# Kernel optimization log

Measured on AMD Instinct MI355X. Metric: run time of the kernel, lower is better.

Reference implementation:

```python
import jax, jax.numpy as jnp
import numpy as np

B, T, N = 1024, 128, 5
HIDDEN = 160
FML = HIDDEN // N            # 32, per-node state width
FC = (256, 256, 512)
IN_F = (FML + 1) * N         # 165: full graph -> every node sees all 5 nodes
N_CLASSES = 7
BN_EPS = 1e-5


def setup_inputs() -> dict:
    key = jax.random.key(0)
    ks = jax.random.split(key, 12)
    init = lambda k, sh: (jax.random.normal(k, sh, jnp.float32) * 0.02)
    return {
        "x": jax.random.normal(ks[0], (B, N, T), jnp.float32),
        # per-node 3-layer MLP f_i, stacked over nodes
        "Wf1": init(ks[1], (N, IN_F, FC[0])), "bf1": jnp.zeros((N, FC[0]), jnp.float32),
        "Wf2": init(ks[2], (N, FC[0], FC[1])), "bf2": jnp.zeros((N, FC[1]), jnp.float32),
        "Wf3": init(ks[3], (N, FC[1], FML)), "bf3": jnp.zeros((N, FML), jnp.float32),
        # output head: Linear -> ReLU -> BatchNorm1d -> Linear -> Softmax
        "Wo1": init(ks[4], (IN_F, FC[2])), "bo1": jnp.zeros((FC[2],), jnp.float32),
        "gamma": jnp.ones((FC[2],), jnp.float32), "beta": jnp.zeros((FC[2],), jnp.float32),
        "Wo2": init(ks[5], (FC[2], N_CLASSES)), "bo2": jnp.zeros((N_CLASSES,), jnp.float32),
    }


def reference(x, Wf1, bf1, Wf2, bf2, Wf3, bf3, Wo1, bo1, gamma, beta, Wo2, bo2):
    batch = x.shape[0]
    xt = jnp.transpose(x, (2, 0, 1))                  # [T, B, N]
    state0 = jnp.zeros((batch, N, FML), x.dtype)      # [B, N, FML]

    def step(state, x_t):
        # Gauss-Seidel update: node i sees states already updated this step
        for i in range(N):
            inp = jnp.concatenate([x_t, state.reshape(batch, -1)], axis=1)  # [B, 165]
            h = jax.nn.relu(inp @ Wf1[i] + bf1[i])
            h = jax.nn.relu(h @ Wf2[i] + bf2[i])
            s_i = jax.nn.relu(h @ Wf3[i] + bf3[i])    # [B, FML]
            state = state.at[:, i, :].set(s_i)
        return state, None

    state, _ = jax.lax.scan(step, state0, xt)
    feat = jnp.concatenate([xt[-1], state.reshape(batch, -1)], axis=1)       # [B, 165]
    h = jax.nn.relu(feat @ Wo1 + bo1)
    # BatchNorm1d in training mode: batch mean, biased batch variance
    mu = jnp.mean(h, axis=0)
    var = jnp.mean((h - mu) ** 2, axis=0)
    h = (h - mu) / jnp.sqrt(var + BN_EPS) * gamma + beta
    logits = h @ Wo2 + bo2
    return jax.nn.softmax(logits, axis=1)             # [B, 7]
```

## Files before the change

kernel.cpp:

```cpp
#include <hip/hip_runtime.h>
#include <hip/hip_bf16.h>

#define B_TOT 1024
#define T_STEPS 128
#define N_NODES 5
#define FML 32
#define IN_F 165
#define F1 256
#define F2 256
#define F3 512
#define NCLS 7
#define BM 16
#define BMH 8

typedef __attribute__((ext_vector_type(8))) short bfrag;
typedef __attribute__((ext_vector_type(4))) float f32x4;

#define MFMA16 __builtin_amdgcn_mfma_f32_16x16x32_bf16

#define P1_NODE 43008
#define P1_XOFF 40960
#define L2_FRAGS 128
#define P2_NODE (L2_FRAGS * 64 * 8)
#define L3_FRAGS 16
#define P3_NODE (L3_FRAGS * 64 * 8)

#define INP_STRIDE 200
#define H_STRIDE 264

__device__ __forceinline__ __hip_bfloat16 tobf(float v) { return __float2bfloat16(v); }

__device__ __forceinline__ void phase_barrier() {
  asm volatile("s_waitcnt lgkmcnt(0)" ::: "memory");
  __builtin_amdgcn_s_barrier();
  __builtin_amdgcn_sched_barrier(0);
}

__global__ __launch_bounds__(256) void pack_weights(
    const float* __restrict__ Wf1, const float* __restrict__ Wf2, const float* __restrict__ Wf3,
    __hip_bfloat16* __restrict__ p1, __hip_bfloat16* __restrict__ p2, __hip_bfloat16* __restrict__ p3) {
  const int stride = gridDim.x * 256;
  for (int it = blockIdx.x * 256 + threadIdx.x; it < N_NODES * 14592; it += stride) {
    int node = it / 14592, u = it % 14592;
    if (u < 5120) {
      int lane = u & 63, frag = u >> 6;
      int kt = frag >> 4, ct = frag & 15;
      int g = lane >> 4, c16 = lane & 15;
      __hip_bfloat16* dst = p1 + (size_t)node * P1_NODE + (size_t)u * 8;
      const float* W = Wf1 + (size_t)node * IN_F * F1;
#pragma unroll
      for (int e = 0; e < 8; ++e) {
        int k = kt * 32 + g * 8 + e;
        dst[e] = tobf(W[(size_t)(5 + k) * F1 + ct * 16 + c16]);
      }
    } else if (u < 5376) {
      int v = u - 5120;
      int ct = v >> 4, c16 = v & 15;
      __hip_bfloat16* dst = p1 + (size_t)node * P1_NODE + P1_XOFF + (size_t)v * 8;
      const float* W = Wf1 + (size_t)node * IN_F * F1;
#pragma unroll
      for (int e = 0; e < 8; ++e)
        dst[e] = (e < 5) ? tobf(W[(size_t)e * F1 + ct * 16 + c16]) : tobf(0.f);
    } else if (u < 5376 + 8192) {
      int v = u - 5376;
      int lane = v & 63, frag = v >> 6;
      int kt = frag >> 4, ct = frag & 15;
      int g = lane >> 4, c16 = lane & 15;
      __hip_bfloat16* dst = p2 + (size_t)node * P2_NODE + (size_t)v * 8;
      const float* W = Wf2 + (size_t)node * F1 * F2;
#pragma unroll
      for (int e = 0; e < 8; ++e) {
        int k = kt * 32 + g * 8 + e;
        dst[e] = tobf(W[(size_t)k * F2 + ct * 16 + c16]);
      }
    } else {
      int v = u - 13568;
      int lane = v & 63, frag = v >> 6;
      int kt = frag >> 1, ct = frag & 1;
      int g = lane >> 4, c16 = lane & 15;
      __hip_bfloat16* dst = p3 + (size_t)node * P3_NODE + (size_t)v * 8;
      const float* W = Wf3 + (size_t)node * F2 * FML;
#pragma unroll
      for (int e = 0; e < 8; ++e) {
        int k = kt * 32 + g * 8 + e;
        dst[e] = tobf(W[(size_t)k * FML + ct * 16 + c16]);
      }
    }
  }
}

__device__ __forceinline__ void relu_pack_store(__hip_bfloat16* p, f32x4 acc, float4 b) {
  union { ushort4 v; __hip_bfloat16 h[4]; } u;
  u.h[0] = tobf(fmaxf(acc[0] + b.x, 0.f));
  u.h[1] = tobf(fmaxf(acc[1] + b.y, 0.f));
  u.h[2] = tobf(fmaxf(acc[2] + b.z, 0.f));
  u.h[3] = tobf(fmaxf(acc[3] + b.w, 0.f));
  *reinterpret_cast<ushort4*>(p) = u.v;
}

__global__ __launch_bounds__(1024, 4) void recur_kernel(
    const float* __restrict__ x,
    const __hip_bfloat16* __restrict__ p1, const float* __restrict__ bf1,
    const __hip_bfloat16* __restrict__ p2, const float* __restrict__ bf2,
    const __hip_bfloat16* __restrict__ p3, const float* __restrict__ bf3,
    float* __restrict__ feat_out) {
  __shared__ __align__(16) __hip_bfloat16 inp_s[BM][INP_STRIDE];
  __shared__ __align__(16) __hip_bfloat16 h1_s[BM][H_STRIDE];
  __shared__ __align__(16) __hip_bfloat16 h2_s[BM][H_STRIDE];
  __shared__ __align__(16) bfrag wf3_s[N_NODES * L3_FRAGS * 64];

  const int tid = threadIdx.x;
  const int lane = tid & 63;
  const int w = tid >> 6;
  const int g = lane >> 4;
  const int c16 = lane & 15;
  const int ct = w;
  const int r0 = blockIdx.x * BM;

  const bfrag* Pf1 = (const bfrag*)p1;
  const bfrag* Pf2 = (const bfrag*)p2;

  {
    const uint4* src = (const uint4*)p3;
    uint4* dst = (uint4*)wf3_s;
    for (int i2 = tid; i2 < N_NODES * L3_FRAGS * 64; i2 += 1024) dst[i2] = src[i2];
  }
  for (int idx = tid; idx < BM * INP_STRIDE; idx += 1024)
    ((__hip_bfloat16*)inp_s)[idx] = tobf(0.f);
  __syncthreads();
  if (tid < BM * N_NODES) {
    int r = tid / N_NODES, n = tid % N_NODES;
    inp_s[r][160 + n] = tobf(x[(size_t)(r0 + r) * (N_NODES * T_STEPS) + n * T_STEPS]);
  }
  __syncthreads();

  bfrag wL1[5], wL1x;
#pragma unroll
  for (int kt = 0; kt < 5; ++kt)
    wL1[kt] = Pf1[(size_t)0 * (P1_NODE / 8) + (kt * 16 + ct) * 64 + lane];
  {
    bfrag z = {0,0,0,0,0,0,0,0};
    wL1x = (g == 0) ? Pf1[(size_t)0 * (P1_NODE / 8) + P1_XOFF / 8 + ct * 16 + c16] : z;
  }

#pragma unroll 1
  for (int t = 0; t < T_STEPS; ++t) {
#pragma unroll 1
    for (int i = 0; i < N_NODES; ++i) {
      const int inext = (i + 1 == N_NODES) ? 0 : i + 1;

      bfrag w2[8];
      {
        const bfrag* P = Pf2 + (size_t)i * L2_FRAGS * 64;
#pragma unroll
        for (int kt = 0; kt < 8; ++kt)
          w2[kt] = P[(kt * 16 + ct) * 64 + lane];
      }
      {
        float4 bia = *(const float4*)&bf1[i * F1 + ct * 16 + 4 * g];
        bfrag a[5], a5;
#pragma unroll
        for (int kt = 0; kt < 5; ++kt)
          a[kt] = *(const bfrag*)&inp_s[c16][kt * 32 + g * 8];
        a5 = *(const bfrag*)&inp_s[c16][160 + g * 8];
        f32x4 acc = {0.f,0.f,0.f,0.f}, accb = {0.f,0.f,0.f,0.f};
        acc  = MFMA16(wL1[0], a[0], acc,  0, 0, 0);
        accb = MFMA16(wL1[3], a[3], accb, 0, 0, 0);
        acc  = MFMA16(wL1[1], a[1], acc,  0, 0, 0);
        accb = MFMA16(wL1[4], a[4], accb, 0, 0, 0);
        acc  = MFMA16(wL1[2], a[2], acc,  0, 0, 0);
        accb = MFMA16(wL1x,   a5,   accb, 0, 0, 0);
        acc += accb;
        relu_pack_store(&h1_s[c16][ct * 16 + 4 * g], acc, bia);
      }
      phase_barrier();

      bfrag w1n[5], w1nx;
      {
        const bfrag* P = Pf1 + (size_t)inext * (P1_NODE / 8);
#pragma unroll
        for (int kt = 0; kt < 5; ++kt)
          w1n[kt] = P[(kt * 16 + ct) * 64 + lane];
        bfrag z = {0,0,0,0,0,0,0,0};
        w1nx = (g == 0) ? P[P1_XOFF / 8 + ct * 16 + c16] : z;
      }
      {
        float4 bib = *(const float4*)&bf2[i * F2 + ct * 16 + 4 * g];
        bfrag ab[8];
#pragma unroll
        for (int kt = 0; kt < 8; ++kt)
          ab[kt] = *(const bfrag*)&h1_s[c16][kt * 32 + g * 8];
        f32x4 acc = {0.f,0.f,0.f,0.f}, accb = {0.f,0.f,0.f,0.f};
#pragma unroll
        for (int kt = 0; kt < 4; ++kt) {
          acc  = MFMA16(w2[kt],     ab[kt],     acc,  0, 0, 0);
          accb = MFMA16(w2[kt + 4], ab[kt + 4], accb, 0, 0, 0);
        }
        acc += accb;
        relu_pack_store(&h2_s[c16][ct * 16 + 4 * g], acc, bib);
      }
      phase_barrier();

      if (w < 2) {
        bfrag ac[8], wc[8];
#pragma unroll
        for (int kt = 0; kt < 8; ++kt) {
          wc[kt] = wf3_s[((size_t)i * L3_FRAGS + kt * 2 + w) * 64 + lane];
          ac[kt] = *(const bfrag*)&h2_s[c16][kt * 32 + g * 8];
        }
        f32x4 acc = {0.f,0.f,0.f,0.f}, accb = {0.f,0.f,0.f,0.f};
#pragma unroll
        for (int kt = 0; kt < 4; ++kt) {
          acc  = MFMA16(wc[kt],     ac[kt],     acc,  0, 0, 0);
          accb = MFMA16(wc[kt + 4], ac[kt + 4], accb, 0, 0, 0);
        }
        acc += accb;
        const int sc = i * FML + w * 16 + 4 * g;
        float4 bic = *(const float4*)&bf3[sc];
        union { ushort4 v; __hip_bfloat16 h[4]; } u;
        float vs[4];
#pragma unroll
        for (int e = 0; e < 4; ++e) {
          vs[e] = fmaxf(acc[e] + ((const float*)&bic)[e], 0.f);
          u.h[e] = tobf(vs[e]);
        }
        *reinterpret_cast<ushort4*>(&inp_s[c16][sc]) = u.v;
        if (t == T_STEPS - 1) {
#pragma unroll
          for (int e = 0; e < 4; ++e)
            feat_out[(size_t)(r0 + c16) * IN_F + 5 + sc + e] = vs[e];
        }
      } else if (i == N_NODES - 1 && t + 1 < T_STEPS && tid >= 512 && tid < 512 + BM * N_NODES) {
        int xr = (tid - 512) / N_NODES, xn = (tid - 512) % N_NODES;
        float xv = x[(size_t)(r0 + xr) * (N_NODES * T_STEPS) + xn * T_STEPS + (t + 1)];
        inp_s[xr][160 + xn] = tobf(xv);
      }
      phase_barrier();

#pragma unroll
      for (int kt = 0; kt < 5; ++kt) wL1[kt] = w1n[kt];
      wL1x = w1nx;
    }
  }

  if (tid < BM * N_NODES) {
    int r = tid / N_NODES, n = tid % N_NODES;
    feat_out[(size_t)(r0 + r) * IN_F + n] =
        x[(size_t)(r0 + r) * (N_NODES * T_STEPS) + n * T_STEPS + (T_STEPS - 1)];
  }
}

__global__ __launch_bounds__(256) void head1_kernel(
    const float* __restrict__ feat, const float* __restrict__ Wo1,
    const float* __restrict__ bo1, float* __restrict__ H) {
  __shared__ __align__(16) float f[BMH][168];
  const int tid = threadIdx.x;
  const int r0 = blockIdx.x * BMH;
  for (int idx = tid; idx < BMH * 168; idx += 256) {
    int r = idx / 168, c = idx % 168;
    f[r][c] = (c < IN_F) ? feat[(size_t)(r0 + r) * IN_F + c] : 0.f;
  }
  __syncthreads();
  const int c0 = tid, c1 = tid + 256;
  float acc0[BMH], acc1[BMH];
#pragma unroll
  for (int r = 0; r < BMH; ++r) { acc0[r] = 0.f; acc1[r] = 0.f; }
  int k = 0;
  for (; k + 3 < IN_F; k += 4) {
    float w00 = Wo1[(k + 0) * F3 + c0], w01 = Wo1[(k + 0) * F3 + c1];
    float w10 = Wo1[(k + 1) * F3 + c0], w11 = Wo1[(k + 1) * F3 + c1];
    float w20 = Wo1[(k + 2) * F3 + c0], w21 = Wo1[(k + 2) * F3 + c1];
    float w30 = Wo1[(k + 3) * F3 + c0], w31 = Wo1[(k + 3) * F3 + c1];
#pragma unroll
    for (int r = 0; r < BMH; ++r) {
      float4 v = *reinterpret_cast<const float4*>(&f[r][k]);
      acc0[r] = fmaf(v.x, w00, acc0[r]); acc1[r] = fmaf(v.x, w01, acc1[r]);
      acc0[r] = fmaf(v.y, w10, acc0[r]); acc1[r] = fmaf(v.y, w11, acc1[r]);
      acc0[r] = fmaf(v.z, w20, acc0[r]); acc1[r] = fmaf(v.z, w21, acc1[r]);
      acc0[r] = fmaf(v.w, w30, acc0[r]); acc1[r] = fmaf(v.w, w31, acc1[r]);
    }
  }
  {
    float w0 = Wo1[164 * F3 + c0], w1 = Wo1[164 * F3 + c1];
#pragma unroll
    for (int r = 0; r < BMH; ++r) {
      acc0[r] = fmaf(f[r][164], w0, acc0[r]);
      acc1[r] = fmaf(f[r][164], w1, acc1[r]);
    }
  }
  float b0 = bo1[c0], b1 = bo1[c1];
#pragma unroll
  for (int r = 0; r < BMH; ++r) {
    H[(size_t)(r0 + r) * F3 + c0] = fmaxf(acc0[r] + b0, 0.f);
    H[(size_t)(r0 + r) * F3 + c1] = fmaxf(acc1[r] + b1, 0.f);
  }
}

__global__ __launch_bounds__(256) void bn_stats_kernel(
    const float* __restrict__ H, const float* __restrict__ gamma,
    const float* __restrict__ beta, float* __restrict__ ab) {
  const int c = blockIdx.x;
  const int tid = threadIdx.x;
  float sm = 0.f, q = 0.f;
  for (int r = tid; r < B_TOT; r += 256) {
    float v = H[(size_t)r * F3 + c];
    sm += v; q += v * v;
  }
  __shared__ float ls[256], lq[256];
  ls[tid] = sm; lq[tid] = q;
  __syncthreads();
  for (int off = 128; off; off >>= 1) {
    if (tid < off) { ls[tid] += ls[tid + off]; lq[tid] += lq[tid + off]; }
    __syncthreads();
  }
  if (tid == 0) {
    float mu = ls[0] * (1.f / B_TOT);
    float var = lq[0] * (1.f / B_TOT) - mu * mu;
    float inv = rsqrtf(var + 1e-5f);
    float a = gamma[c] * inv;
    ab[c] = a;
    ab[F3 + c] = beta[c] - mu * a;
  }
}

__global__ __launch_bounds__(256) void out_kernel(
    const float* __restrict__ H, const float* __restrict__ ab,
    const float* __restrict__ Wo2, const float* __restrict__ bo2,
    float* __restrict__ out) {
  const int wid = threadIdx.x >> 6, lane = threadIdx.x & 63;
  const int r = blockIdx.x * 4 + wid;
  float acc[NCLS];
#pragma unroll
  for (int j = 0; j < NCLS; ++j) acc[j] = 0.f;
  for (int k = lane; k < F3; k += 64) {
    float hv = H[(size_t)r * F3 + k] * ab[k] + ab[F3 + k];
#pragma unroll
    for (int j = 0; j < NCLS; ++j) acc[j] = fmaf(hv, Wo2[k * NCLS + j], acc[j]);
  }
#pragma unroll
  for (int j = 0; j < NCLS; ++j)
    for (int off = 32; off; off >>= 1) acc[j] += __shfl_xor(acc[j], off);
  if (lane == 0) {
    float lg[NCLS], mx = -1e30f;
#pragma unroll
    for (int j = 0; j < NCLS; ++j) { lg[j] = acc[j] + bo2[j]; mx = fmaxf(mx, lg[j]); }
    float sum = 0.f;
#pragma unroll
    for (int j = 0; j < NCLS; ++j) { lg[j] = __expf(lg[j] - mx); sum += lg[j]; }
    float inv = 1.f / sum;
#pragma unroll
    for (int j = 0; j < NCLS; ++j) out[(size_t)r * NCLS + j] = lg[j] * inv;
  }
}

extern "C" void kernel_launch(void* const* d_in, const int* in_sizes, int n_in,
                              void* d_out, int out_size, void* d_ws, size_t ws_size,
                              hipStream_t stream) {
  const float* x   = (const float*)d_in[0];
  const float* Wf1 = (const float*)d_in[1];
  const float* bf1 = (const float*)d_in[2];
  const float* Wf2 = (const float*)d_in[3];
  const float* bf2 = (const float*)d_in[4];
  const float* Wf3 = (const float*)d_in[5];
  const float* bf3 = (const float*)d_in[6];
  const float* Wo1 = (const float*)d_in[7];
  const float* bo1 = (const float*)d_in[8];
  const float* gamma = (const float*)d_in[9];
  const float* beta  = (const float*)d_in[10];
  const float* Wo2 = (const float*)d_in[11];
  const float* bo2 = (const float*)d_in[12];
  float* out = (float*)d_out;

  char* ws = (char*)d_ws;
  size_t off = 0;
  __hip_bfloat16* p1 = (__hip_bfloat16*)(ws + off); off += (size_t)N_NODES * P1_NODE * 2;
  __hip_bfloat16* p2 = (__hip_bfloat16*)(ws + off); off += (size_t)N_NODES * P2_NODE * 2;
  __hip_bfloat16* p3 = (__hip_bfloat16*)(ws + off); off += (size_t)N_NODES * P3_NODE * 2;
  float* feat = (float*)(ws + off); off += (size_t)B_TOT * IN_F * 4;
  float* H    = (float*)(ws + off); off += (size_t)B_TOT * F3 * 4;
  float* ab   = (float*)(ws + off); off += 2 * F3 * 4;

  pack_weights<<<285, 256, 0, stream>>>(Wf1, Wf2, Wf3, p1, p2, p3);
  recur_kernel<<<B_TOT / BM, 1024, 0, stream>>>(x, p1, bf1, p2, bf2, p3, bf3, feat);
  head1_kernel<<<B_TOT / BMH, 256, 0, stream>>>(feat, Wo1, bo1, H);
  bn_stats_kernel<<<F3, 256, 0, stream>>>(H, gamma, beta, ab);
  out_kernel<<<B_TOT / 4, 256, 0, stream>>>(H, ab, Wo2, bo2, out);
}
```

Measured before the change: 1.569 ms.

## Enlarge batch tile to 64 rows with 8 waves each computing two column tiles

The recurrent kernel now processes 64 batch rows per block with 512 threads, where each wave holds weight fragments for two output column tiles and reuses them across four 16-row tiles. This amortizes per-step global weight-fragment loads over four times as many rows, but cuts the grid from 64 to 16 blocks, leaving most CUs idle on a 256-CU GPU. Layer-3 weights are now read from global memory instead of staged in shared memory, and the custom phase barrier is replaced by __syncthreads.

Result: slower. 2.546 ms (+62.3%).

```diff
diff --git a/kernel.cpp b/kernel.cpp
--- a/kernel.cpp
+++ b/kernel.cpp
@@ -10,7 +10,8 @@
 #define F2 256
 #define F3 512
 #define NCLS 7
-#define BM 16
+#define BM 64
+#define NRT 4
 #define BMH 8
 
 typedef __attribute__((ext_vector_type(8))) short bfrag;
@@ -29,12 +30,6 @@
 #define H_STRIDE 264
 
 __device__ __forceinline__ __hip_bfloat16 tobf(float v) { return __float2bfloat16(v); }
-
-__device__ __forceinline__ void phase_barrier() {
-  asm volatile("s_waitcnt lgkmcnt(0)" ::: "memory");
-  __builtin_amdgcn_s_barrier();
-  __builtin_amdgcn_sched_barrier(0);
-}
 
 __global__ __launch_bounds__(256) void pack_weights(
     const float* __restrict__ Wf1, const float* __restrict__ Wf2, const float* __restrict__ Wf3,
@@ -98,7 +93,7 @@
   *reinterpret_cast<ushort4*>(p) = u.v;
 }
 
-__global__ __launch_bounds__(1024, 4) void recur_kernel(
+__global__ __launch_bounds__(512, 2) void recur_kernel(
     const float* __restrict__ x,
     const __hip_bfloat16* __restrict__ p1, const float* __restrict__ bf1,
     const __hip_bfloat16* __restrict__ p2, const float* __restrict__ bf2,
@@ -107,25 +102,20 @@
   __shared__ __align__(16) __hip_bfloat16 inp_s[BM][INP_STRIDE];
   __shared__ __align__(16) __hip_bfloat16 h1_s[BM][H_STRIDE];
   __shared__ __align__(16) __hip_bfloat16 h2_s[BM][H_STRIDE];
-  __shared__ __align__(16) bfrag wf3_s[N_NODES * L3_FRAGS * 64];
 
   const int tid = threadIdx.x;
   const int lane = tid & 63;
   const int w = tid >> 6;
   const int g = lane >> 4;
   const int c16 = lane & 15;
-  const int ct = w;
+  const int ct0 = 2 * w, ct1 = 2 * w + 1;
   const int r0 = blockIdx.x * BM;
 
   const bfrag* Pf1 = (const bfrag*)p1;
   const bfrag* Pf2 = (const bfrag*)p2;
-
-  {
-    const uint4* src = (const uint4*)p3;
-    uint4* dst = (uint4*)wf3_s;
-    for (int i2 = tid; i2 < N_NODES * L3_FRAGS * 64; i2 += 1024) dst[i2] = src[i2];
-  }
-  for (int idx = tid; idx < BM * INP_STRIDE; idx += 1024)
+  const bfrag* Pf3 = (const bfrag*)p3;
+
+  for (int idx = tid; idx < BM * INP_STRIDE; idx += 512)
     ((__hip_bfloat16*)inp_s)[idx] = tobf(0.f);
   __syncthreads();
   if (tid < BM * N_NODES) {
@@ -134,13 +124,16 @@
   }
   __syncthreads();
 
-  bfrag wL1[5], wL1x;
-#pragma unroll
-  for (int kt = 0; kt < 5; ++kt)
-    wL1[kt] = Pf1[(size_t)0 * (P1_NODE / 8) + (kt * 16 + ct) * 64 + lane];
+  bfrag wL1[2][5], wL1x[2];
+#pragma unroll
+  for (int kt = 0; kt < 5; ++kt) {
+    wL1[0][kt] = Pf1[(kt * 16 + ct0) * 64 + lane];
+    wL1[1][kt] = Pf1[(kt * 16 + ct1) * 64 + lane];
+  }
   {
     bfrag z = {0,0,0,0,0,0,0,0};
-    wL1x = (g == 0) ? Pf1[(size_t)0 * (P1_NODE / 8) + P1_XOFF / 8 + ct * 16 + c16] : z;
+    wL1x[0] = (g == 0) ? Pf1[P1_XOFF / 8 + ct0 * 16 + c16] : z;
+    wL1x[1] = (g == 0) ? Pf1[P1_XOFF / 8 + ct1 * 16 + c16] : z;
   }
 
 #pragma unroll 1
@@ -149,73 +142,110 @@
     for (int i = 0; i < N_NODES; ++i) {
       const int inext = (i + 1 == N_NODES) ? 0 : i + 1;
 
-      bfrag w2[8];
+      bfrag w2[2][8];
       {
         const bfrag* P = Pf2 + (size_t)i * L2_FRAGS * 64;
 #pragma unroll
-        for (int kt = 0; kt < 8; ++kt)
-          w2[kt] = P[(kt * 16 + ct) * 64 + lane];
+        for (int kt = 0; kt < 8; ++kt) {
+          w2[0][kt] = P[(kt * 16 + ct0) * 64 + lane];
+          w2[1][kt] = P[(kt * 16 + ct1) * 64 + lane];
+        }
       }
       {
-        float4 bia = *(const float4*)&bf1[i * F1 + ct * 16 + 4 * g];
-        bfrag a[5], a5;
-#pragma unroll
-        for (int kt = 0; kt < 5; ++kt)
-          a[kt] = *(const bfrag*)&inp_s[c16][kt * 32 + g * 8];
-        a5 = *(const bfrag*)&inp_s[c16][160 + g * 8];
-        f32x4 acc = {0.f,0.f,0.f,0.f}, accb = {0.f,0.f,0.f,0.f};
-        acc  = MFMA16(wL1[0], a[0], acc,  0, 0, 0);
-        accb = MFMA16(wL1[3], a[3], accb, 0, 0, 0);
-        acc  = MFMA16(wL1[1], a[1], acc,  0, 0, 0);
-        accb = MFMA16(wL1[4], a[4], accb, 0, 0, 0);
-        acc  = MFMA16(wL1[2], a[2], acc,  0, 0, 0);
-        accb = MFMA16(wL1x,   a5,   accb, 0, 0, 0);
-        acc += accb;
-        relu_pack_store(&h1_s[c16][ct * 16 + 4 * g], acc, bia);
-      }
-      phase_barrier();
-
-      bfrag w1n[5], w1nx;
+        float4 biA0 = *(const float4*)&bf1[i * F1 + ct0 * 16 + 4 * g];
+        float4 biA1 = *(const float4*)&bf1[i * F1 + ct1 * 16 + 4 * g];
+#pragma unroll
+        for (int rt = 0; rt < NRT; ++rt) {
+          const int row = rt * 16 + c16;
+          bfrag a[5], a5;
+#pragma unroll
+          for (int kt = 0; kt < 5; ++kt)
+            a[kt] = *(const bfrag*)&inp_s[row][kt * 32 + g * 8];
+          a5 = *(const bfrag*)&inp_s[row][160 + g * 8];
+          f32x4 acc0 = {0.f,0.f,0.f,0.f}, acc1 = {0.f,0.f,0.f,0.f};
+          f32x4 acc0b = {0.f,0.f,0.f,0.f}, acc1b = {0.f,0.f,0.f,0.f};
+#pragma unroll
+          for (int kt = 0; kt < 2; ++kt) {
+            acc0  = MFMA16(wL1[0][kt],     a[kt],     acc0,  0, 0, 0);
+            acc1  = MFMA16(wL1[1][kt],     a[kt],     acc1,  0, 0, 0);
+            acc0b = MFMA16(wL1[0][kt + 2], a[kt + 2], acc0b, 0, 0, 0);
+            acc1b = MFMA16(wL1[1][kt + 2], a[kt + 2], acc1b, 0, 0, 0);
+          }
+          acc0  = MFMA16(wL1[0][4], a[4], acc0,  0, 0, 0);
+          acc1  = MFMA16(wL1[1][4], a[4], acc1,  0, 0, 0);
+          acc0b = MFMA16(wL1x[0],   a5,   acc0b, 0, 0, 0);
+          acc1b = MFMA16(wL1x[1],   a5,   acc1b, 0, 0, 0);
+          acc0 += acc0b; acc1 += acc1b;
+          relu_pack_store(&h1_s[row][ct0 * 16 + 4 * g], acc0, biA0);
+          relu_pack_store(&h1_s[row][ct1 * 16 + 4 * g], acc1, biA1);
+        }
+      }
+      __syncthreads();
+
+      bfrag w1n[2][5], w1nx[2];
       {
         const bfrag* P = Pf1 + (size_t)inext * (P1_NODE / 8);
 #pragma unroll
-        for (int kt = 0; kt < 5; ++kt)
-          w1n[kt] = P[(kt * 16 + ct) * 64 + lane];
+        for (int kt = 0; kt < 5; ++kt) {
+          w1n[0][kt] = P[(kt * 16 + ct0) * 64 + lane];
+          w1n[1][kt] = P[(kt * 16 + ct1) * 64 + lane];
+        }
         bfrag z = {0,0,0,0,0,0,0,0};
-        w1nx = (g == 0) ? P[P1_XOFF / 8 + ct * 16 + c16] : z;
-      }
+        w1nx[0] = (g == 0) ? P[P1_XOFF / 8 + ct0 * 16 + c16] : z;
+        w1nx[1] = (g == 0) ? P[P1_XOFF / 8 + ct1 * 16 + c16] : z;
+      }
+      float xv = 0.f;
+      if (i == 4 && tid < BM * N_NODES && t + 1 < T_STEPS)
+        xv = x[(size_t)(r0 + tid / N_NODES) * (N_NODES * T_STEPS) +
+               (tid % N_NODES) * T_STEPS + (t + 1)];
       {
-        float4 bib = *(const float4*)&bf2[i * F2 + ct * 16 + 4 * g];
-        bfrag ab[8];
+        float4 biB0 = *(const float4*)&bf2[i * F2 + ct0 * 16 + 4 * g];
+        float4 biB1 = *(const float4*)&bf2[i * F2 + ct1 * 16 + 4 * g];
+#pragma unroll
+        for (int rt = 0; rt < NRT; ++rt) {
+          const int row = rt * 16 + c16;
+          bfrag ab[8];
+#pragma unroll
+          for (int kt = 0; kt < 8; ++kt)
+            ab[kt] = *(const bfrag*)&h1_s[row][kt * 32 + g * 8];
+          f32x4 acc0 = {0.f,0.f,0.f,0.f}, acc1 = {0.f,0.f,0.f,0.f};
+          f32x4 acc0b = {0.f,0.f,0.f,0.f}, acc1b = {0.f,0.f,0.f,0.f};
+#pragma unroll
+          for (int kt = 0; kt < 4; ++kt) {
+            acc0  = MFMA16(w2[0][kt],     ab[kt],     acc0,  0, 0, 0);
+            acc1  = MFMA16(w2[1][kt],     ab[kt],     acc1,  0, 0, 0);
+            acc0b = MFMA16(w2[0][kt + 4], ab[kt + 4], acc0b, 0, 0, 0);
+            acc1b = MFMA16(w2[1][kt + 4], ab[kt + 4], acc1b, 0, 0, 0);
+          }
+          acc0 += acc0b; acc1 += acc1b;
+          relu_pack_store(&h2_s[row][ct0 * 16 + 4 * g], acc0, biB0);
+          relu_pack_store(&h2_s[row][ct1 * 16 + 4 * g], acc1, biB1);
+        }
+      }
+      __syncthreads();
+
+      {
+        const int rt = w >> 1, ctc = w & 1;
+        const int row = rt * 16 + c16;
+        bfrag w3[8];
+        {
+          const bfrag* P = Pf3 + (size_t)i * L3_FRAGS * 64;
+#pragma unroll
+          for (int kt = 0; kt < 8; ++kt)
+            w3[kt] = P[(kt * 2 + ctc) * 64 + lane];
+        }
+        bfrag ac[8];
 #pragma unroll
         for (int kt = 0; kt < 8; ++kt)
-          ab[kt] = *(const bfrag*)&h1_s[c16][kt * 32 + g * 8];
+          ac[kt] = *(const bfrag*)&h2_s[row][kt * 32 + g * 8];
         f32x4 acc = {0.f,0.f,0.f,0.f}, accb = {0.f,0.f,0.f,0.f};
 #pragma unroll
         for (int kt = 0; kt < 4; ++kt) {
-          acc  = MFMA16(w2[kt],     ab[kt],     acc,  0, 0, 0);
-          accb = MFMA16(w2[kt + 4], ab[kt + 4], accb, 0, 0, 0);
+          acc  = MFMA16(w3[kt],     ac[kt],     acc,  0, 0, 0);
+          accb = MFMA16(w3[kt + 4], ac[kt + 4], accb, 0, 0, 0);
         }
         acc += accb;
-        relu_pack_store(&h2_s[c16][ct * 16 + 4 * g], acc, bib);
-      }
-      phase_barrier();
-
-      if (w < 2) {
-        bfrag ac[8], wc[8];
-#pragma unroll
-        for (int kt = 0; kt < 8; ++kt) {
-          wc[kt] = wf3_s[((size_t)i * L3_FRAGS + kt * 2 + w) * 64 + lane];
-          ac[kt] = *(const bfrag*)&h2_s[c16][kt * 32 + g * 8];
-        }
-        f32x4 acc = {0.f,0.f,0.f,0.f}, accb = {0.f,0.f,0.f,0.f};
-#pragma unroll
-        for (int kt = 0; kt < 4; ++kt) {
-          acc  = MFMA16(wc[kt],     ac[kt],     acc,  0, 0, 0);
-          accb = MFMA16(wc[kt + 4], ac[kt + 4], accb, 0, 0, 0);
-        }
-        acc += accb;
-        const int sc = i * FML + w * 16 + 4 * g;
+        const int sc = i * FML + ctc * 16 + 4 * g;
         float4 bic = *(const float4*)&bf3[sc];
         union { ushort4 v; __hip_bfloat16 h[4]; } u;
         float vs[4];
@@ -224,22 +254,24 @@
           vs[e] = fmaxf(acc[e] + ((const float*)&bic)[e], 0.f);
           u.h[e] = tobf(vs[e]);
         }
-        *reinterpret_cast<ushort4*>(&inp_s[c16][sc]) = u.v;
+        *reinterpret_cast<ushort4*>(&inp_s[row][sc]) = u.v;
         if (t == T_STEPS - 1) {
 #pragma unroll
           for (int e = 0; e < 4; ++e)
-            feat_out[(size_t)(r0 + c16) * IN_F + 5 + sc + e] = vs[e];
-        }
-      } else if (i == N_NODES - 1 && t + 1 < T_STEPS && tid >= 512 && tid < 512 + BM * N_NODES) {
-        int xr = (tid - 512) / N_NODES, xn = (tid - 512) % N_NODES;
-        float xv = x[(size_t)(r0 + xr) * (N_NODES * T_STEPS) + xn * T_STEPS + (t + 1)];
-        inp_s[xr][160 + xn] = tobf(xv);
-      }
-      phase_barrier();
-
-#pragma unroll
-      for (int kt = 0; kt < 5; ++kt) wL1[kt] = w1n[kt];
-      wL1x = w1nx;
+            feat_out[(size_t)(r0 + row) * IN_F + 5 + sc + e] = vs[e];
+        }
+      }
+      if (i == 4 && tid < BM * N_NODES && t + 1 < T_STEPS)
+        inp_s[tid / N_NODES][160 + tid % N_NODES] = tobf(xv);
+      __syncthreads();
+
+#pragma unroll
+      for (int kt = 0; kt < 5; ++kt) {
+        wL1[0][kt] = w1n[0][kt];
+        wL1[1][kt] = w1n[1][kt];
+      }
+      wL1x[0] = w1nx[0];
+      wL1x[1] = w1nx[1];
     }
   }
 
@@ -381,7 +413,7 @@
   float* ab   = (float*)(ws + off); off += 2 * F3 * 4;
 
   pack_weights<<<285, 256, 0, stream>>>(Wf1, Wf2, Wf3, p1, p2, p3);
-  recur_kernel<<<B_TOT / BM, 1024, 0, stream>>>(x, p1, bf1, p2, bf2, p3, bf3, feat);
+  recur_kernel<<<B_TOT / BM, 512, 0, stream>>>(x, p1, bf1, p2, bf2, p3, bf3, feat);
   head1_kernel<<<B_TOT / BMH, 256, 0, stream>>>(feat, Wo1, bo1, H);
   bn_stats_kernel<<<F3, 256, 0, stream>>>(H, gamma, beta, ab);
   out_kernel<<<B_TOT / 4, 256, 0, stream>>>(H, ab, Wo2, bo2, out);
```
